# Kernel optimization log

Hardware: AMD Instinct MI355X
Metric: run time of the kernel (lower is better)

Reference implementation:

```python
import jax, jax.numpy as jnp
import numpy as np

N_NODES = 100000
N_EDGES = 1600000
NODE_IN = 32
HID = 64
EDGE_IN = 8


def _glorot(key, shape):
    fan_in = shape[0]
    return jax.random.normal(key, shape, jnp.float32) * (1.0 / np.sqrt(fan_in))


def setup_inputs() -> dict:
    key = jax.random.key(0)
    ks = jax.random.split(key, 16)
    d = {}
    d["x"] = jax.random.normal(ks[0], (N_NODES, NODE_IN), jnp.float32)
    d["edge_index"] = jax.random.randint(ks[1], (2, N_EDGES), 0, N_NODES, dtype=jnp.int32)
    d["edge_attr"] = jax.random.normal(ks[2], (N_EDGES, EDGE_IN), jnp.float32)
    # SAGEConv layers: lin_l (aggregated neighbors, with bias), lin_r (root, no bias)
    d["Wl0"] = _glorot(ks[3], (NODE_IN, HID)); d["bl0"] = jnp.zeros((HID,), jnp.float32)
    d["Wr0"] = _glorot(ks[4], (NODE_IN, HID))
    d["Wl1"] = _glorot(ks[5], (HID, HID)); d["bl1"] = jnp.zeros((HID,), jnp.float32)
    d["Wr1"] = _glorot(ks[6], (HID, HID))
    d["Wl2"] = _glorot(ks[7], (HID, HID)); d["bl2"] = jnp.zeros((HID,), jnp.float32)
    d["Wr2"] = _glorot(ks[8], (HID, HID))
    # Edge predictor MLP: (2*HID + EDGE_IN) -> 64 -> 32 -> 1
    pin = 2 * HID + EDGE_IN
    d["W1"] = _glorot(ks[9], (pin, 64)); d["b1"] = jnp.zeros((64,), jnp.float32)
    d["W2"] = _glorot(ks[10], (64, 32)); d["b2"] = jnp.zeros((32,), jnp.float32)
    d["W3"] = _glorot(ks[11], (32, 1)); d["b3"] = jnp.zeros((1,), jnp.float32)
    return d


def _sage_mean(h, src, dst, Wl, bl, Wr):
    # PyG SAGEConv(aggr='mean'): lin_l(mean_{j->i} x_j) + lin_r(x_i)
    n = h.shape[0]
    summed = jax.ops.segment_sum(h[src], dst, num_segments=n)  # [N, F]
    cnt = jax.ops.segment_sum(jnp.ones((src.shape[0], 1), h.dtype), dst, num_segments=n)
    mean = summed / jnp.maximum(cnt, 1.0)
    return mean @ Wl + bl + h @ Wr


def reference(x, edge_index, edge_attr,
              Wl0, bl0, Wr0, Wl1, bl1, Wr1, Wl2, bl2, Wr2,
              W1, b1, W2, b2, W3, b3):
    src, dst = edge_index[0], edge_index[1]
    h = _sage_mean(x, src, dst, Wl0, bl0, Wr0)
    h = jax.nn.relu(h)  # dropout inactive (eval mode)
    h = _sage_mean(h, src, dst, Wl1, bl1, Wr1)
    h = jax.nn.relu(h)
    h = _sage_mean(h, src, dst, Wl2, bl2, Wr2)
    # Edge-level predictor: gather endpoint embeddings + edge features
    edge_repr = jnp.concatenate([h[src], h[dst], edge_attr], axis=1)  # [E, 2*HID+EDGE_IN]
    z = jax.nn.relu(edge_repr @ W1 + b1)
    z = jax.nn.relu(z @ W2 + b2)
    return jax.nn.sigmoid(z @ W3 + b3)  # [E, 1]
```

## Files before the change

kernel.cpp:

```cpp
#include <hip/hip_runtime.h>
#include <hip/hip_bf16.h>

#define NN 100000
#define NE 1600000
#define HID 64
#define SCAN_BS 256
#define NBLK ((NN + SCAN_BS - 1) / SCAN_BS)

typedef float f32x4 __attribute__((ext_vector_type(4)));
typedef short bf16x8 __attribute__((ext_vector_type(8)));

__device__ __forceinline__ float bflo(unsigned u) { return __uint_as_float(u << 16); }
__device__ __forceinline__ float bfhi(unsigned u) { return __uint_as_float(u & 0xffff0000u); }
__device__ __forceinline__ unsigned short f2bf(float f) {
    __hip_bfloat16 h = (__hip_bfloat16)f;
    return *(unsigned short*)&h;
}

__global__ void xcast(const float* __restrict__ in, unsigned short* __restrict__ out, int n4) {
    int i = blockIdx.x * blockDim.x + threadIdx.x;
    if (i >= n4) return;
    float4 v = ((const float4*)in)[i];
    ushort4 o;
    o.x = f2bf(v.x); o.y = f2bf(v.y); o.z = f2bf(v.z); o.w = f2bf(v.w);
    ((ushort4*)out)[i] = o;
}

__global__ void count_kernel(const int* __restrict__ dst, int* __restrict__ degI, int nE) {
    int e = blockIdx.x * blockDim.x + threadIdx.x;
    if (e < nE) atomicAdd(&degI[dst[e]], 1);
}

__global__ void scan1_kernel(const int* __restrict__ degI, int* __restrict__ rowtmp,
                             int* __restrict__ blockSum) {
    __shared__ int tmp[SCAN_BS];
    int t = threadIdx.x;
    int i = blockIdx.x * SCAN_BS + t;
    int d = (i < NN) ? degI[i] : 0;
    tmp[t] = d;
    __syncthreads();
    for (int off = 1; off < SCAN_BS; off <<= 1) {
        int v = (t >= off) ? tmp[t - off] : 0;
        __syncthreads();
        tmp[t] += v;
        __syncthreads();
    }
    if (i < NN) rowtmp[i] = tmp[t] - d;
    if (t == SCAN_BS - 1) blockSum[blockIdx.x] = tmp[t];
}

__global__ void scan2_kernel(const int* __restrict__ blockSum, int* __restrict__ blockOff, int n) {
    __shared__ int tmp[512];
    int t = threadIdx.x;
    tmp[t] = (t < n) ? blockSum[t] : 0;
    __syncthreads();
    for (int off = 1; off < 512; off <<= 1) {
        int v = (t >= off) ? tmp[t - off] : 0;
        __syncthreads();
        tmp[t] += v;
        __syncthreads();
    }
    if (t < n) blockOff[t] = (t == 0) ? 0 : tmp[t - 1];
}

__global__ void scan3_kernel(const int* __restrict__ rowtmp, const int* __restrict__ blockOff,
                             int* __restrict__ row_ptr) {
    int i = blockIdx.x * SCAN_BS + threadIdx.x;
    if (i < NN) row_ptr[i] = rowtmp[i] + blockOff[blockIdx.x];
}

__global__ void fill_kernel(const int* __restrict__ src, const int* __restrict__ dst,
                            const int* __restrict__ row_ptr, int* __restrict__ cursor,
                            int* __restrict__ csr_src, int nE) {
    int e = blockIdx.x * blockDim.x + threadIdx.x;
    if (e >= nE) return;
    int d = dst[e];
    int pos = atomicAdd(&cursor[d], 1);
    csr_src[row_ptr[d] + pos] = src[e];
}

template <int IN>
__launch_bounds__(256)
__global__ void aggregate(const int* __restrict__ row_ptr, const int* __restrict__ degI,
                          const int* __restrict__ csr_src,
                          const unsigned short* __restrict__ hin,
                          float* __restrict__ mout) {
    constexpr int LPE = IN / 4;
    constexpr int SPLIT = 64 / LPE;
    constexpr int UN = (SPLIT >= 8) ? 2 : 4;
    int g = threadIdx.x >> 6;
    int lane = threadIdx.x & 63;
    int node = blockIdx.x * 4 + g;
    int lane_p = lane & (LPE - 1);
    int sub = lane / LPE;

    float a0 = 0.f, a1 = 0.f, a2 = 0.f, a3 = 0.f;
    int start = row_ptr[node];
    int dg = degI[node];
    const int* cs = csr_src + start;

    int e = sub;
    for (; e + SPLIT * (UN - 1) < dg; e += SPLIT * UN) {
        int sidx[UN];
#pragma unroll
        for (int j = 0; j < UN; ++j) sidx[j] = cs[e + SPLIT * j];
        uint2 u[UN];
#pragma unroll
        for (int j = 0; j < UN; ++j)
            u[j] = *(const uint2*)(hin + (size_t)sidx[j] * IN + 4 * lane_p);
#pragma unroll
        for (int j = 0; j < UN; ++j) {
            a0 += bflo(u[j].x); a1 += bfhi(u[j].x);
            a2 += bflo(u[j].y); a3 += bfhi(u[j].y);
        }
    }
    for (; e < dg; e += SPLIT) {
        uint2 u = *(const uint2*)(hin + (size_t)cs[e] * IN + 4 * lane_p);
        a0 += bflo(u.x); a1 += bfhi(u.x);
        a2 += bflo(u.y); a3 += bfhi(u.y);
    }

#pragma unroll
    for (int m = LPE; m < 64; m <<= 1) {
        a0 += __shfl_xor(a0, m);
        a1 += __shfl_xor(a1, m);
        a2 += __shfl_xor(a2, m);
        a3 += __shfl_xor(a3, m);
    }
    if (sub == 0) {
        float r = 1.0f / fmaxf((float)dg, 1.0f);
        float4 v;
        v.x = a0 * r; v.y = a1 * r; v.z = a2 * r; v.w = a3 * r;
        *(float4*)(mout + (size_t)node * IN + 4 * lane_p) = v;
    }
}

__global__ void wprep(const float* __restrict__ Wl0, const float* __restrict__ Wr0,
                      const float* __restrict__ Wl1, const float* __restrict__ Wr1,
                      const float* __restrict__ Wl2, const float* __restrict__ Wr2,
                      const float* __restrict__ W1, unsigned short* __restrict__ out) {
    int b = blockIdx.x;
    int mid, local;
    if (b < 2) { mid = b; local = 0; }
    else { mid = 2 + (b - 2) / 2; local = (b - 2) & 1; }
    const float* Ws[8] = {Wl0, Wr0, Wl1, Wr1, Wl2, Wr2, W1, W1 + 64 * 64};
    const int offs[8] = {0, 4096, 8192, 16384, 24576, 32768, 40960, 49152};
    const float* W = Ws[mid];
    int e = local * 256 + threadIdx.x;
    int lane = e & 63;
    int fi = e >> 6;
    int ks = fi >> 2, nt = fi & 3;
    int lg = lane >> 4, col = lane & 15;
    unsigned short hi[8], lo[8];
#pragma unroll
    for (int j = 0; j < 8; ++j) {
        float w = W[(ks * 32 + lg * 8 + j) * 64 + nt * 16 + col];
        unsigned short h = f2bf(w);
        hi[j] = h;
        lo[j] = f2bf(w - bflo(h));
    }
    unsigned short* dh = out + offs[mid] + ((size_t)(fi * 2 + 0) * 64 + lane) * 8;
    unsigned short* dl = out + offs[mid] + ((size_t)(fi * 2 + 1) * 64 + lane) * 8;
#pragma unroll
    for (int j = 0; j < 8; ++j) { dh[j] = hi[j]; dl[j] = lo[j]; }
}

template <int KIN, bool RELU>
__launch_bounds__(256)
__global__ void sage_gemm(const float* __restrict__ meanv,
                          const unsigned short* __restrict__ hroot,
                          const unsigned short* __restrict__ wl_pk,
                          const unsigned short* __restrict__ wr_pk,
                          const float* __restrict__ bl,
                          unsigned short* __restrict__ hout) {
    constexpr int NKS = KIN / 32;
    int wid = threadIdx.x >> 6, lane = threadIdx.x & 63;
    int tile = blockIdx.x * 4 + wid;
    if (tile >= NN / 16) return;
    int m0 = tile * 16;
    int ar = lane & 15;
    int lg = lane >> 4;

    bf16x8 ah[NKS];
#pragma unroll
    for (int ks = 0; ks < NKS; ++ks)
        ah[ks] = *(const bf16x8*)(hroot + (size_t)(m0 + ar) * KIN + ks * 32 + lg * 8);

    bf16x8 amh[NKS], aml[NKS];
#pragma unroll
    for (int ks = 0; ks < NKS; ++ks) {
        const float* p = meanv + (size_t)(m0 + ar) * KIN + ks * 32 + lg * 8;
        float4 v0 = *(const float4*)p;
        float4 v1 = *(const float4*)(p + 4);
        float mv[8] = {v0.x, v0.y, v0.z, v0.w, v1.x, v1.y, v1.z, v1.w};
#pragma unroll
        for (int j = 0; j < 8; ++j) {
            unsigned short h = f2bf(mv[j]);
            amh[ks][j] = (short)h;
            aml[ks][j] = (short)f2bf(mv[j] - bflo(h));
        }
    }

#pragma unroll
    for (int nt = 0; nt < 4; ++nt) {
        f32x4 acc = {0.f, 0.f, 0.f, 0.f};
#pragma unroll
        for (int ks = 0; ks < NKS; ++ks) {
            int fi = ks * 4 + nt;
            bf16x8 wlh = *(const bf16x8*)(wl_pk + ((size_t)(fi * 2 + 0) * 64 + lane) * 8);
            bf16x8 wll = *(const bf16x8*)(wl_pk + ((size_t)(fi * 2 + 1) * 64 + lane) * 8);
            bf16x8 wrh = *(const bf16x8*)(wr_pk + ((size_t)(fi * 2 + 0) * 64 + lane) * 8);
            bf16x8 wrl = *(const bf16x8*)(wr_pk + ((size_t)(fi * 2 + 1) * 64 + lane) * 8);
            acc = __builtin_amdgcn_mfma_f32_16x16x32_bf16(amh[ks], wlh, acc, 0, 0, 0);
            acc = __builtin_amdgcn_mfma_f32_16x16x32_bf16(amh[ks], wll, acc, 0, 0, 0);
            acc = __builtin_amdgcn_mfma_f32_16x16x32_bf16(aml[ks], wlh, acc, 0, 0, 0);
            acc = __builtin_amdgcn_mfma_f32_16x16x32_bf16(ah[ks],  wrh, acc, 0, 0, 0);
            acc = __builtin_amdgcn_mfma_f32_16x16x32_bf16(ah[ks],  wrl, acc, 0, 0, 0);
        }
        float b = bl[nt * 16 + ar];
#pragma unroll
        for (int r = 0; r < 4; ++r) {
            float o = acc[r] + b;
            if (RELU) o = fmaxf(o, 0.f);
            hout[(size_t)(m0 + lg * 4 + r) * 64 + nt * 16 + ar] = f2bf(o);
        }
    }
}

__launch_bounds__(256)
__global__ void pred_gemm(const unsigned short* __restrict__ h2,
                          const unsigned short* __restrict__ wa_pk,
                          const unsigned short* __restrict__ wb_pk,
                          unsigned short* __restrict__ a1,
                          unsigned short* __restrict__ a2) {
    int wid = threadIdx.x >> 6, lane = threadIdx.x & 63;
    int tile = blockIdx.x * 4 + wid;
    if (tile >= NN / 16) return;
    int m0 = tile * 16;
    int ar = lane & 15;
    int lg = lane >> 4;
    bf16x8 ah[2];
#pragma unroll
    for (int ks = 0; ks < 2; ++ks)
        ah[ks] = *(const bf16x8*)(h2 + (size_t)(m0 + ar) * 64 + ks * 32 + lg * 8);
#pragma unroll
    for (int nt = 0; nt < 4; ++nt) {
        f32x4 p = {0.f, 0.f, 0.f, 0.f};
        f32x4 q = {0.f, 0.f, 0.f, 0.f};
#pragma unroll
        for (int ks = 0; ks < 2; ++ks) {
            int fi = ks * 4 + nt;
            bf16x8 wah = *(const bf16x8*)(wa_pk + ((size_t)(fi * 2 + 0) * 64 + lane) * 8);
            bf16x8 wal = *(const bf16x8*)(wa_pk + ((size_t)(fi * 2 + 1) * 64 + lane) * 8);
            bf16x8 wbh = *(const bf16x8*)(wb_pk + ((size_t)(fi * 2 + 0) * 64 + lane) * 8);
            bf16x8 wbl = *(const bf16x8*)(wb_pk + ((size_t)(fi * 2 + 1) * 64 + lane) * 8);
            p = __builtin_amdgcn_mfma_f32_16x16x32_bf16(ah[ks], wah, p, 0, 0, 0);
            p = __builtin_amdgcn_mfma_f32_16x16x32_bf16(ah[ks], wal, p, 0, 0, 0);
            q = __builtin_amdgcn_mfma_f32_16x16x32_bf16(ah[ks], wbh, q, 0, 0, 0);
            q = __builtin_amdgcn_mfma_f32_16x16x32_bf16(ah[ks], wbl, q, 0, 0, 0);
        }
#pragma unroll
        for (int r = 0; r < 4; ++r) {
            size_t off = (size_t)(m0 + lg * 4 + r) * 64 + nt * 16 + ar;
            a1[off] = f2bf(p[r]);
            a2[off] = f2bf(q[r]);
        }
    }
}

__launch_bounds__(256)
__global__ void edge_pred(const int* __restrict__ src, const int* __restrict__ dst,
                          const unsigned short* __restrict__ a1, const unsigned short* __restrict__ a2,
                          const float* __restrict__ ea,
                          const float* __restrict__ W1, const float* __restrict__ b1,
                          const float* __restrict__ W2, const float* __restrict__ b2,
                          const float* __restrict__ W3, const float* __restrict__ b3,
                          float* __restrict__ out, int nE) {
    int e = blockIdx.x * blockDim.x + threadIdx.x;
    if (e >= nE) return;
    int s = src[e];
    int d = dst[e];

    const uint4* pa = (const uint4*)(a1 + (size_t)s * 64);
    const uint4* pb = (const uint4*)(a2 + (size_t)d * 64);
    const float4* eav = (const float4*)(ea + (size_t)e * 8);
    float4 v0 = eav[0];
    float4 v1 = eav[1];

    float z1[64];
    const float* wr = W1 + 128 * 64;
#pragma unroll
    for (int j = 0; j < 64; ++j) {
        float a = fmaf(v0.x, wr[j], b1[j]);
        a = fmaf(v0.y, wr[64 + j], a);
        a = fmaf(v0.z, wr[128 + j], a);
        a = fmaf(v0.w, wr[192 + j], a);
        a = fmaf(v1.x, wr[256 + j], a);
        a = fmaf(v1.y, wr[320 + j], a);
        a = fmaf(v1.z, wr[384 + j], a);
        z1[j] = fmaf(v1.w, wr[448 + j], a);
    }

#pragma unroll
    for (int q = 0; q < 8; ++q) {
        uint4 ua = pa[q];
        uint4 ub = pb[q];
        int j0 = q * 8;
        z1[j0 + 0] += bflo(ua.x) + bflo(ub.x);
        z1[j0 + 1] += bfhi(ua.x) + bfhi(ub.x);
        z1[j0 + 2] += bflo(ua.y) + bflo(ub.y);
        z1[j0 + 3] += bfhi(ua.y) + bfhi(ub.y);
        z1[j0 + 4] += bflo(ua.z) + bflo(ub.z);
        z1[j0 + 5] += bfhi(ua.z) + bfhi(ub.z);
        z1[j0 + 6] += bflo(ua.w) + bflo(ub.w);
        z1[j0 + 7] += bfhi(ua.w) + bfhi(ub.w);
    }

    float z2[32];
#pragma unroll
    for (int j = 0; j < 32; ++j) z2[j] = b2[j];
    for (int k = 0; k < 64; ++k) {
        float v = fmaxf(z1[k], 0.0f);
        const float* w = W2 + (size_t)k * 32;
#pragma unroll
        for (int j = 0; j < 32; ++j) z2[j] = fmaf(v, w[j], z2[j]);
    }

    float o = b3[0];
#pragma unroll
    for (int k = 0; k < 32; ++k) o = fmaf(fmaxf(z2[k], 0.0f), W3[k], o);

    out[e] = 1.0f / (1.0f + __expf(-o));
}

extern "C" void kernel_launch(void* const* d_in, const int* in_sizes, int n_in,
                              void* d_out, int out_size, void* d_ws, size_t ws_size,
                              hipStream_t stream) {
    const float* x   = (const float*)d_in[0];
    const int*   ei  = (const int*)d_in[1];
    const float* ea  = (const float*)d_in[2];
    const float* Wl0 = (const float*)d_in[3];
    const float* bl0 = (const float*)d_in[4];
    const float* Wr0 = (const float*)d_in[5];
    const float* Wl1 = (const float*)d_in[6];
    const float* bl1 = (const float*)d_in[7];
    const float* Wr1 = (const float*)d_in[8];
    const float* Wl2 = (const float*)d_in[9];
    const float* bl2 = (const float*)d_in[10];
    const float* Wr2 = (const float*)d_in[11];
    const float* W1  = (const float*)d_in[12];
    const float* b1  = (const float*)d_in[13];
    const float* W2  = (const float*)d_in[14];
    const float* b2  = (const float*)d_in[15];
    const float* W3  = (const float*)d_in[16];
    const float* b3  = (const float*)d_in[17];

    const int* src = ei;
    const int* dst = ei + NE;

    char* ws = (char*)d_ws;
    size_t off = 0;
    auto alloc = [&](size_t bytes) {
        void* p = ws + off;
        off += (bytes + 255) & ~(size_t)255;
        return p;
    };
    unsigned short* xb = (unsigned short*)alloc((size_t)NN * 32 * 2);
    unsigned short* hA = (unsigned short*)alloc((size_t)NN * HID * 2);
    unsigned short* hB = (unsigned short*)alloc((size_t)NN * HID * 2);
    unsigned short* a1 = (unsigned short*)alloc((size_t)NN * HID * 2);
    unsigned short* a2 = (unsigned short*)alloc((size_t)NN * HID * 2);
    unsigned short* wpk = (unsigned short*)alloc((size_t)57344 * 2);
    int* degI    = (int*)alloc(NN * sizeof(int));
    int* row_ptr = (int*)alloc(NN * sizeof(int));
    int* rowtmp  = (int*)alloc(NN * sizeof(int));
    int* cursor  = (int*)alloc(NN * sizeof(int));
    int* blockSum= (int*)alloc(512 * sizeof(int));
    int* blockOff= (int*)alloc(512 * sizeof(int));
    int* csr_src = (int*)alloc((size_t)NE * sizeof(int));
    float* meanv = (float*)a1;
    float* out = (float*)d_out;

    const int BS = 256;
    dim3 blkE((NE + BS - 1) / BS);
    int n4 = NN * 32 / 4;
    int gemm_blk = (NN / 16 + 3) / 4;

    hipMemsetAsync(degI, 0, NN * sizeof(int), stream);
    hipMemsetAsync(cursor, 0, NN * sizeof(int), stream);
    xcast<<<(n4 + BS - 1) / BS, BS, 0, stream>>>(x, xb, n4);
    count_kernel<<<blkE, BS, 0, stream>>>(dst, degI, NE);
    scan1_kernel<<<NBLK, SCAN_BS, 0, stream>>>(degI, rowtmp, blockSum);
    scan2_kernel<<<1, 512, 0, stream>>>(blockSum, blockOff, NBLK);
    scan3_kernel<<<NBLK, SCAN_BS, 0, stream>>>(rowtmp, blockOff, row_ptr);
    fill_kernel<<<blkE, BS, 0, stream>>>(src, dst, row_ptr, cursor, csr_src, NE);
    wprep<<<14, 256, 0, stream>>>(Wl0, Wr0, Wl1, Wr1, Wl2, Wr2, W1, wpk);

    aggregate<32><<<NN / 4, 256, 0, stream>>>(row_ptr, degI, csr_src, xb, meanv);
    sage_gemm<32, true><<<gemm_blk, 256, 0, stream>>>(meanv, xb, wpk + 0, wpk + 4096, bl0, hA);
    aggregate<64><<<NN / 4, 256, 0, stream>>>(row_ptr, degI, csr_src, hA, meanv);
    sage_gemm<64, true><<<gemm_blk, 256, 0, stream>>>(meanv, hA, wpk + 8192, wpk + 16384, bl1, hB);
    aggregate<64><<<NN / 4, 256, 0, stream>>>(row_ptr, degI, csr_src, hB, meanv);
    sage_gemm<64, false><<<gemm_blk, 256, 0, stream>>>(meanv, hB, wpk + 24576, wpk + 32768, bl2, hA);
    pred_gemm<<<gemm_blk, 256, 0, stream>>>(hA, wpk + 40960, wpk + 49152, a1, a2);

    edge_pred<<<blkE, BS, 0, stream>>>(src, dst, a1, a2, ea, W1, b1, W2, b2, W3, b3, out, NE);
}
```

Before: 560.8 us.

## Move edge predictor MLP onto bf16 MFMA with split-precision weights

Rewrites the per-edge predictor so each wavefront handles 16 edges and computes the edge-attribute projection and the 64->32 layer with bf16 MFMA instructions. A new prep kernel packs the W1 edge rows, the biases and W2 into hi/lo bf16 fragments so the split-bf16 products keep near-fp32 accuracy. This replaces the scalar per-thread FMA chains and the large per-thread z1/z2 register arrays. In exchange it adds an extra tiny launch, several more MFMAs per tile, and a cross-lane shuffle reduction for the final dot product.

```diff
diff --git a/kernel.cpp b/kernel.cpp
--- a/kernel.cpp
+++ b/kernel.cpp
@@ -165,6 +165,72 @@
     for (int j = 0; j < 8; ++j) { dh[j] = hi[j]; dl[j] = lo[j]; }
 }
 
+__global__ void wprep2(const float* __restrict__ W1, const float* __restrict__ b1,
+                       const float* __restrict__ W2, const float* __restrict__ b2,
+                       unsigned short* __restrict__ we_pk,
+                       unsigned short* __restrict__ w2h_pk,
+                       unsigned short* __restrict__ w2l_pk) {
+    int t = threadIdx.x;
+    const float* W1e = W1 + 128 * 64;
+    {
+        int mt = t >> 6, lane = t & 63;
+        int ar = lane & 15, lg = lane >> 4;
+        int f = mt * 16 + ar;
+        unsigned short v[8];
+#pragma unroll
+        for (int j = 0; j < 8; ++j) {
+            if (lg <= 1) {
+                v[j] = f2bf(W1e[j * 64 + f]);
+            } else if (lg == 2) {
+                float w = W1e[j * 64 + f];
+                unsigned short h = f2bf(w);
+                v[j] = f2bf(w - bflo(h));
+            } else {
+                if (j == 0) v[j] = f2bf(b1[f]);
+                else if (j == 1) {
+                    float bb = b1[f];
+                    unsigned short h = f2bf(bb);
+                    v[j] = f2bf(bb - bflo(h));
+                } else v[j] = 0;
+            }
+        }
+        unsigned short* o = we_pk + (size_t)t * 8;
+        for (int j = 0; j < 8; ++j) o[j] = v[j];
+    }
+    for (int i = t; i < 640; i += 256) {
+        int mt2 = i / 320, rem = i % 320;
+        int ks = rem >> 6, lane = rem & 63;
+        int ar = lane & 15, lg = lane >> 4;
+        int c = mt2 * 16 + ar;
+        unsigned short v[8] = {0, 0, 0, 0, 0, 0, 0, 0};
+        if (ks < 4) {
+            for (int j = 0; j < 4; ++j)
+                v[j] = f2bf(W2[(ks * 16 + lg * 4 + j) * 32 + c]);
+        } else if (lg == 0) {
+            float bb = b2[c];
+            unsigned short h = f2bf(bb);
+            v[0] = h;
+            v[1] = f2bf(bb - bflo(h));
+        }
+        unsigned short* o = w2h_pk + (size_t)i * 8;
+        for (int j = 0; j < 8; ++j) o[j] = v[j];
+    }
+    for (int i = t; i < 512; i += 256) {
+        int mt2 = i / 256, rem = i % 256;
+        int ks = rem >> 6, lane = rem & 63;
+        int ar = lane & 15, lg = lane >> 4;
+        int c = mt2 * 16 + ar;
+        unsigned short v[8] = {0, 0, 0, 0, 0, 0, 0, 0};
+        for (int j = 0; j < 4; ++j) {
+            float w = W2[(ks * 16 + lg * 4 + j) * 32 + c];
+            unsigned short h = f2bf(w);
+            v[j] = f2bf(w - bflo(h));
+        }
+        unsigned short* o = w2l_pk + (size_t)i * 8;
+        for (int j = 0; j < 8; ++j) o[j] = v[j];
+    }
+}
+
 template <int KIN, bool RELU>
 __launch_bounds__(256)
 __global__ void sage_gemm(const float* __restrict__ meanv,
@@ -272,65 +338,99 @@
 __global__ void edge_pred(const int* __restrict__ src, const int* __restrict__ dst,
                           const unsigned short* __restrict__ a1, const unsigned short* __restrict__ a2,
                           const float* __restrict__ ea,
-                          const float* __restrict__ W1, const float* __restrict__ b1,
-                          const float* __restrict__ W2, const float* __restrict__ b2,
+                          const unsigned short* __restrict__ we_pk,
+                          const unsigned short* __restrict__ w2h_pk,
+                          const unsigned short* __restrict__ w2l_pk,
                           const float* __restrict__ W3, const float* __restrict__ b3,
-                          float* __restrict__ out, int nE) {
-    int e = blockIdx.x * blockDim.x + threadIdx.x;
-    if (e >= nE) return;
+                          float* __restrict__ out) {
+    int wid = threadIdx.x >> 6, lane = threadIdx.x & 63;
+    int tile = blockIdx.x * 4 + wid;
+    int e0 = tile * 16;
+    int ar = lane & 15, lg = lane >> 4;
+    int e = e0 + ar;
+
     int s = src[e];
     int d = dst[e];
 
-    const uint4* pa = (const uint4*)(a1 + (size_t)s * 64);
-    const uint4* pb = (const uint4*)(a2 + (size_t)d * 64);
-    const float4* eav = (const float4*)(ea + (size_t)e * 8);
-    float4 v0 = eav[0];
-    float4 v1 = eav[1];
-
-    float z1[64];
-    const float* wr = W1 + 128 * 64;
-#pragma unroll
-    for (int j = 0; j < 64; ++j) {
-        float a = fmaf(v0.x, wr[j], b1[j]);
-        a = fmaf(v0.y, wr[64 + j], a);
-        a = fmaf(v0.z, wr[128 + j], a);
-        a = fmaf(v0.w, wr[192 + j], a);
-        a = fmaf(v1.x, wr[256 + j], a);
-        a = fmaf(v1.y, wr[320 + j], a);
-        a = fmaf(v1.z, wr[384 + j], a);
-        z1[j] = fmaf(v1.w, wr[448 + j], a);
-    }
-
-#pragma unroll
-    for (int q = 0; q < 8; ++q) {
-        uint4 ua = pa[q];
-        uint4 ub = pb[q];
-        int j0 = q * 8;
-        z1[j0 + 0] += bflo(ua.x) + bflo(ub.x);
-        z1[j0 + 1] += bfhi(ua.x) + bfhi(ub.x);
-        z1[j0 + 2] += bflo(ua.y) + bflo(ub.y);
-        z1[j0 + 3] += bfhi(ua.y) + bfhi(ub.y);
-        z1[j0 + 4] += bflo(ua.z) + bflo(ub.z);
-        z1[j0 + 5] += bfhi(ua.z) + bfhi(ub.z);
-        z1[j0 + 6] += bflo(ua.w) + bflo(ub.w);
-        z1[j0 + 7] += bfhi(ua.w) + bfhi(ub.w);
-    }
-
-    float z2[32];
-#pragma unroll
-    for (int j = 0; j < 32; ++j) z2[j] = b2[j];
-    for (int k = 0; k < 64; ++k) {
-        float v = fmaxf(z1[k], 0.0f);
-        const float* w = W2 + (size_t)k * 32;
-#pragma unroll
-        for (int j = 0; j < 32; ++j) z2[j] = fmaf(v, w[j], z2[j]);
-    }
-
-    float o = b3[0];
-#pragma unroll
-    for (int k = 0; k < 32; ++k) o = fmaf(fmaxf(z2[k], 0.0f), W3[k], o);
-
-    out[e] = 1.0f / (1.0f + __expf(-o));
+    const float4* ep = (const float4*)(ea + (size_t)e * 8);
+    float4 f0 = ep[0], f1 = ep[1];
+    float ev[8] = {f0.x, f0.y, f0.z, f0.w, f1.x, f1.y, f1.z, f1.w};
+    bf16x8 bea = {0, 0, 0, 0, 0, 0, 0, 0};
+    if (lg == 3) {
+        bea[0] = (short)0x3F80; bea[1] = (short)0x3F80;
+    } else if (lg == 1) {
+#pragma unroll
+        for (int j = 0; j < 8; ++j) {
+            unsigned short h = f2bf(ev[j]);
+            bea[j] = (short)f2bf(ev[j] - bflo(h));
+        }
+    } else {
+#pragma unroll
+        for (int j = 0; j < 8; ++j) bea[j] = (short)f2bf(ev[j]);
+    }
+
+    uint2 ua[4], ub[4];
+#pragma unroll
+    for (int ks = 0; ks < 4; ++ks) {
+        ua[ks] = *(const uint2*)(a1 + (size_t)s * 64 + ks * 16 + lg * 4);
+        ub[ks] = *(const uint2*)(a2 + (size_t)d * 64 + ks * 16 + lg * 4);
+    }
+
+    f32x4 accE[4];
+#pragma unroll
+    for (int mt = 0; mt < 4; ++mt) {
+        bf16x8 aw = *(const bf16x8*)(we_pk + ((size_t)(mt * 64 + lane)) * 8);
+        f32x4 z = {0.f, 0.f, 0.f, 0.f};
+        accE[mt] = __builtin_amdgcn_mfma_f32_16x16x32_bf16(aw, bea, z, 0, 0, 0);
+    }
+
+    f32x4 acc2[2] = {{0.f, 0.f, 0.f, 0.f}, {0.f, 0.f, 0.f, 0.f}};
+#pragma unroll
+    for (int ks = 0; ks < 4; ++ks) {
+        float z0 = accE[ks][0] + bflo(ua[ks].x) + bflo(ub[ks].x);
+        float z1 = accE[ks][1] + bfhi(ua[ks].x) + bfhi(ub[ks].x);
+        float z2 = accE[ks][2] + bflo(ua[ks].y) + bflo(ub[ks].y);
+        float z3 = accE[ks][3] + bfhi(ua[ks].y) + bfhi(ub[ks].y);
+        z0 = fmaxf(z0, 0.f); z1 = fmaxf(z1, 0.f);
+        z2 = fmaxf(z2, 0.f); z3 = fmaxf(z3, 0.f);
+        unsigned short h0 = f2bf(z0), h1 = f2bf(z1), h2 = f2bf(z2), h3 = f2bf(z3);
+        bf16x8 zh = {(short)h0, (short)h1, (short)h2, (short)h3, 0, 0, 0, 0};
+        bf16x8 zl = {(short)f2bf(z0 - bflo(h0)), (short)f2bf(z1 - bflo(h1)),
+                     (short)f2bf(z2 - bflo(h2)), (short)f2bf(z3 - bflo(h3)), 0, 0, 0, 0};
+#pragma unroll
+        for (int mt2 = 0; mt2 < 2; ++mt2) {
+            bf16x8 Ah = *(const bf16x8*)(w2h_pk + ((size_t)((mt2 * 5 + ks) * 64 + lane)) * 8);
+            bf16x8 Al = *(const bf16x8*)(w2l_pk + ((size_t)((mt2 * 4 + ks) * 64 + lane)) * 8);
+            acc2[mt2] = __builtin_amdgcn_mfma_f32_16x16x32_bf16(Ah, zh, acc2[mt2], 0, 0, 0);
+            acc2[mt2] = __builtin_amdgcn_mfma_f32_16x16x32_bf16(Ah, zl, acc2[mt2], 0, 0, 0);
+            acc2[mt2] = __builtin_amdgcn_mfma_f32_16x16x32_bf16(Al, zh, acc2[mt2], 0, 0, 0);
+        }
+    }
+    {
+        bf16x8 bone = {0, 0, 0, 0, 0, 0, 0, 0};
+        if (lg == 0) { bone[0] = (short)0x3F80; bone[1] = (short)0x3F80; }
+#pragma unroll
+        for (int mt2 = 0; mt2 < 2; ++mt2) {
+            bf16x8 Ah = *(const bf16x8*)(w2h_pk + ((size_t)((mt2 * 5 + 4) * 64 + lane)) * 8);
+            acc2[mt2] = __builtin_amdgcn_mfma_f32_16x16x32_bf16(Ah, bone, acc2[mt2], 0, 0, 0);
+        }
+    }
+
+    float p = 0.f;
+#pragma unroll
+    for (int mt2 = 0; mt2 < 2; ++mt2) {
+        float4 w3 = *(const float4*)(W3 + mt2 * 16 + lg * 4);
+        p = fmaf(fmaxf(acc2[mt2][0], 0.f), w3.x, p);
+        p = fmaf(fmaxf(acc2[mt2][1], 0.f), w3.y, p);
+        p = fmaf(fmaxf(acc2[mt2][2], 0.f), w3.z, p);
+        p = fmaf(fmaxf(acc2[mt2][3], 0.f), w3.w, p);
+    }
+    p += __shfl_xor(p, 16);
+    p += __shfl_xor(p, 32);
+    if (lane < 16) {
+        float o = p + b3[0];
+        out[e] = 1.0f / (1.0f + __expf(-o));
+    }
 }
 
 extern "C" void kernel_launch(void* const* d_in, const int* in_sizes, int n_in,
@@ -370,7 +470,7 @@
     unsigned short* hB = (unsigned short*)alloc((size_t)NN * HID * 2);
     unsigned short* a1 = (unsigned short*)alloc((size_t)NN * HID * 2);
     unsigned short* a2 = (unsigned short*)alloc((size_t)NN * HID * 2);
-    unsigned short* wpk = (unsigned short*)alloc((size_t)57344 * 2);
+    unsigned short* wpk = (unsigned short*)alloc((size_t)68608 * 2);
     int* degI    = (int*)alloc(NN * sizeof(int));
     int* row_ptr = (int*)alloc(NN * sizeof(int));
     int* rowtmp  = (int*)alloc(NN * sizeof(int));
@@ -381,6 +481,10 @@
     float* meanv = (float*)a1;
     float* out = (float*)d_out;
 
+    unsigned short* we_pk  = wpk + 57344;
+    unsigned short* w2h_pk = wpk + 59392;
+    unsigned short* w2l_pk = wpk + 64512;
+
     const int BS = 256;
     dim3 blkE((NE + BS - 1) / BS);
     int n4 = NN * 32 / 4;
@@ -395,6 +499,7 @@
     scan3_kernel<<<NBLK, SCAN_BS, 0, stream>>>(rowtmp, blockOff, row_ptr);
     fill_kernel<<<blkE, BS, 0, stream>>>(src, dst, row_ptr, cursor, csr_src, NE);
     wprep<<<14, 256, 0, stream>>>(Wl0, Wr0, Wl1, Wr1, Wl2, Wr2, W1, wpk);
+    wprep2<<<1, 256, 0, stream>>>(W1, b1, W2, b2, we_pk, w2h_pk, w2l_pk);
 
     aggregate<32><<<NN / 4, 256, 0, stream>>>(row_ptr, degI, csr_src, xb, meanv);
     sage_gemm<32, true><<<gemm_blk, 256, 0, stream>>>(meanv, xb, wpk + 0, wpk + 4096, bl0, hA);
@@ -404,5 +509,5 @@
     sage_gemm<64, false><<<gemm_blk, 256, 0, stream>>>(meanv, hB, wpk + 24576, wpk + 32768, bl2, hA);
     pred_gemm<<<gemm_blk, 256, 0, stream>>>(hA, wpk + 40960, wpk + 49152, a1, a2);
 
-    edge_pred<<<blkE, BS, 0, stream>>>(src, dst, a1, a2, ea, W1, b1, W2, b2, W3, b3, out, NE);
-}
+    edge_pred<<<NE / 64, BS, 0, stream>>>(src, dst, a1, a2, ea, we_pk, w2h_pk, w2l_pk, W3, b3, out);
+}
```

After: 633.1 us. 12.9% more time.
